# Kernel optimization log

Measured on AMD Instinct MI355X. Metric: run time of the kernel, lower is better.

The kernel has to match this reference:

```python
import jax, jax.numpy as jnp
import numpy as np

N = 129  # fixed by fc1: 3*121 -> N-8 = 121
F = 262144
E = 16384

def setup_inputs() -> dict:
    key = jax.random.key(0)
    ks = jax.random.split(key, 18)
    s = 0.05
    return {
        "x": jax.random.normal(ks[0], (N, F), jnp.float32),
        "edge_index": jax.random.randint(ks[1], (2, E), 0, N),
        "edge_attr": jax.random.uniform(ks[2], (E, 3), jnp.float32),
        # GCNConvSortPool (channel1 only; forward reuses it for all 3 edge channels)
        "gcn1_W": jax.random.normal(ks[3], (F, 1), jnp.float32) * (1.0 / np.sqrt(F)),
        "gcn1_b": jnp.zeros((1,), jnp.float32),
        "gcn2_W": jax.random.normal(ks[4], (1, 1), jnp.float32),
        "gcn2_b": jnp.zeros((1,), jnp.float32),
        "conv1_w": jax.random.normal(ks[5], (3, 2, 3), jnp.float32) * s,  # OIH
        "conv1_b": jax.random.normal(ks[6], (3,), jnp.float32) * s,
        "conv2_w": jax.random.normal(ks[7], (1, 3, 3), jnp.float32) * s,
        "conv2_b": jax.random.normal(ks[8], (1,), jnp.float32) * s,
        "fc1_W": jax.random.normal(ks[9], (3 * 121, 32), jnp.float32) * s,
        "fc1_b": jnp.zeros((32,), jnp.float32),
        "fc2_W": jax.random.normal(ks[10], (32, 6), jnp.float32) * s,
        "fc2_b": jnp.zeros((6,), jnp.float32),
        "fc3_W": jax.random.normal(ks[11], (6, 2), jnp.float32) * s,
        "fc3_b": jnp.zeros((2,), jnp.float32),
    }

def _gcn_conv(x, row, col, ew, W, b):
    # PyG GCNConv with edge weights: add self loops (weight 1), symmetric norm.
    n = x.shape[0]
    xw = x @ W                                             # [n, out]
    loop = jnp.arange(n)
    row2 = jnp.concatenate([row, loop])
    col2 = jnp.concatenate([col, loop])
    ew2 = jnp.concatenate([ew, jnp.ones((n,), x.dtype)])
    deg = jax.ops.segment_sum(ew2, col2, num_segments=n)
    dinv = jnp.where(deg > 0, deg ** -0.5, 0.0)
    norm = dinv[row2] * ew2 * dinv[col2]                   # [e+n]
    out = jax.ops.segment_sum(norm[:, None] * xw[row2], col2, num_segments=n)
    return out + b

def _maxpool1d3(z):
    return jax.lax.reduce_window(z, -jnp.inf, jax.lax.max, (1, 1, 3), (1, 1, 1), 'VALID')

def _conv1d(z, w, b):
    out = jax.lax.conv_general_dilated(z, w, (1,), 'VALID', dimension_numbers=('NCH', 'OIH', 'NCH'))
    return out + b[None, :, None]

def _channel(x, row, col, ew, gcn1_W, gcn1_b, gcn2_W, gcn2_b, conv1_w, conv1_b, conv2_w, conv2_b):
    h1 = _gcn_conv(x, row, col, ew, gcn1_W, gcn1_b)        # [N,1]
    h2 = _gcn_conv(h1[:, -1:], row, col, ew, gcn2_W, gcn2_b)  # [N,1]
    h = jnp.concatenate([h1, h2], axis=-1)                 # [N,2]
    perm = jnp.argsort(-h[:, -1])                          # SortPool: sort by last channel, descending, k=N
    h = h[perm]                                            # [N,2]
    z = h.T[None]                                          # [1,2,N]
    z = _maxpool1d3(_conv1d(z, conv1_w, conv1_b))          # [1,3,N-4]
    z = _maxpool1d3(_conv1d(z, conv2_w, conv2_b))          # [1,1,N-8]
    return z

def reference(x, edge_index, edge_attr, gcn1_W, gcn1_b, gcn2_W, gcn2_b,
              conv1_w, conv1_b, conv2_w, conv2_b,
              fc1_W, fc1_b, fc2_W, fc2_b, fc3_W, fc3_b):
    row, col = edge_index[0], edge_index[1]
    outs = [_channel(x, row, col, edge_attr[:, c], gcn1_W, gcn1_b, gcn2_W, gcn2_b,
                     conv1_w, conv1_b, conv2_w, conv2_b) for c in range(3)]
    all_x = jnp.concatenate(outs, axis=-2)                 # [1,3,121]
    h = all_x.reshape(1, -1)                               # [1,363]
    h = jax.nn.elu(h @ fc1_W + fc1_b)                      # dropout=0 -> identity
    h = jax.nn.elu(h @ fc2_W + fc2_b)
    return h @ fc3_W + fc3_b                               # [1,2]
```

## Files before the change

### kernel.cpp

```cpp
#include <hip/hip_runtime.h>
#include <hip/hip_bf16.h>
#include <math.h>

#define NN 129
#define FF 262144
#define EE 16384
#define CHUNKS 32
#define CHUNK (FF / CHUNKS)
#define NAGG 16
#define EPB (EE / NAGG)

#define OFF_PARTIAL 0
#define OFF_DEGP    (OFF_PARTIAL + NN*CHUNKS)
#define OFF_DINV    (OFF_DEGP + NAGG*3*NN)
#define OFF_XW      (OFF_DINV + 3*NN)
#define OFF_H1P     (OFF_XW + NN)
#define OFF_H1      (OFF_H1P + NAGG*3*NN)
#define OFF_H2P     (OFF_H1 + 3*NN)

__global__ __launch_bounds__(256) void k_matvec(
    const float* __restrict__ x, const float* __restrict__ W,
    const int* __restrict__ eidx, const float* __restrict__ eattr,
    double* __restrict__ ws)
{
    const int b = blockIdx.x;
    const int tid = threadIdx.x;
    const int wave = tid >> 6, lane = tid & 63;

    __shared__ double ws4[4];
    __shared__ double dp[4][3][NN];

    if (b < NN * CHUNKS) {
        const int r = b / CHUNKS, ch = b % CHUNKS;
        const float4* xp = (const float4*)(x + (size_t)r * FF + (size_t)ch * CHUNK);
        const float4* wp = (const float4*)(W + (size_t)ch * CHUNK);
        double acc = 0.0;
#pragma unroll
        for (int i = 0; i < CHUNK / (256 * 4); ++i) {
            float4 xv = xp[tid + i * 256];
            float4 wv = wp[tid + i * 256];
            acc += (double)xv.x * (double)wv.x + (double)xv.y * (double)wv.y
                 + (double)xv.z * (double)wv.z + (double)xv.w * (double)wv.w;
        }
        for (int off = 32; off > 0; off >>= 1) acc += __shfl_down(acc, off, 64);
        if (lane == 0) ws4[wave] = acc;
        __syncthreads();
        if (tid == 0) ws[OFF_PARTIAL + b] = (ws4[0] + ws4[1]) + (ws4[2] + ws4[3]);
    } else {
        const int bb = b - NN * CHUNKS;
        for (int i = tid; i < 4 * 3 * NN; i += 256) ((double*)dp)[i] = 0.0;
        __syncthreads();
        const int* col = eidx + EE;
#pragma unroll
        for (int i = 0; i < EPB / 256; ++i) {
            const int e = bb * EPB + i * 256 + tid;
            const int cl = col[e];
#pragma unroll
            for (int c = 0; c < 3; ++c)
                unsafeAtomicAdd(&dp[wave][c][cl], (double)eattr[e * 3 + c]);
        }
        __syncthreads();
        for (int i = tid; i < 3 * NN; i += 256)
            ws[OFF_DEGP + bb * (3 * NN) + i] =
                (dp[0][0][0 * 0] , ((dp[0][i / NN][i % NN] + dp[1][i / NN][i % NN])
                                  + (dp[2][i / NN][i % NN] + dp[3][i / NN][i % NN])));
    }
}

__global__ __launch_bounds__(256) void k_reduce1(double* __restrict__ ws)
{
    const int tid = threadIdx.x;
    if (blockIdx.x == 0) {
        for (int j = tid; j < NN; j += 256) {
            double s = 0.0;
#pragma unroll
            for (int k = 0; k < CHUNKS; ++k) s += ws[OFF_PARTIAL + j * CHUNKS + k];
            ws[OFF_XW + j] = s;
        }
    } else {
        for (int v = tid; v < 3 * NN; v += 256) {
            double d = 1.0;
#pragma unroll
            for (int b = 0; b < NAGG; ++b) d += ws[OFF_DEGP + b * (3 * NN) + v];
            ws[OFF_DINV + v] = (d > 0.0) ? 1.0 / sqrt(d) : 0.0;
        }
    }
}

__global__ __launch_bounds__(256) void k_agg1(
    const int* __restrict__ eidx, const float* __restrict__ eattr,
    double* __restrict__ ws)
{
    const int b = blockIdx.x, tid = threadIdx.x, wave = tid >> 6;
    __shared__ double sxw[NN];
    __shared__ double sdinv[3][NN];
    __shared__ double hp[4][3][NN];
    for (int i = tid; i < NN; i += 256) sxw[i] = ws[OFF_XW + i];
    for (int i = tid; i < 3 * NN; i += 256) ((double*)sdinv)[i] = ws[OFF_DINV + i];
    for (int i = tid; i < 4 * 3 * NN; i += 256) ((double*)hp)[i] = 0.0;
    __syncthreads();
    const int* row = eidx;
    const int* col = eidx + EE;
#pragma unroll
    for (int i = 0; i < EPB / 256; ++i) {
        const int e = b * EPB + i * 256 + tid;
        const int r = row[e], cl = col[e];
        const double xwr = sxw[r];
#pragma unroll
        for (int c = 0; c < 3; ++c) {
            const double nw = sdinv[c][r] * (double)eattr[e * 3 + c] * sdinv[c][cl];
            unsafeAtomicAdd(&hp[wave][c][cl], nw * xwr);
        }
    }
    __syncthreads();
    for (int i = tid; i < 3 * NN; i += 256) {
        const int c = i / NN, j = i % NN;
        ws[OFF_H1P + b * (3 * NN) + i] =
            (hp[0][c][j] + hp[1][c][j]) + (hp[2][c][j] + hp[3][c][j]);
    }
}

__global__ __launch_bounds__(256) void k_h1(
    const float* __restrict__ b1, double* __restrict__ ws)
{
    const int tid = threadIdx.x;
    const double bb1 = (double)b1[0];
    for (int i = tid; i < 3 * NN; i += 256) {
        const int j = i % NN;
        const double dv = ws[OFF_DINV + i];
        double s = dv * dv * ws[OFF_XW + j] + bb1;
#pragma unroll
        for (int b = 0; b < NAGG; ++b) s += ws[OFF_H1P + b * (3 * NN) + i];
        ws[OFF_H1 + i] = s;
    }
}

__global__ __launch_bounds__(256) void k_agg2(
    const int* __restrict__ eidx, const float* __restrict__ eattr,
    const float* __restrict__ W2, double* __restrict__ ws)
{
    const int b = blockIdx.x, tid = threadIdx.x, wave = tid >> 6;
    __shared__ double sh1[3][NN];
    __shared__ double sdinv[3][NN];
    __shared__ double hp[4][3][NN];
    const double w2 = (double)W2[0];
    for (int i = tid; i < 3 * NN; i += 256) {
        ((double*)sh1)[i] = ws[OFF_H1 + i];
        ((double*)sdinv)[i] = ws[OFF_DINV + i];
    }
    for (int i = tid; i < 4 * 3 * NN; i += 256) ((double*)hp)[i] = 0.0;
    __syncthreads();
    const int* row = eidx;
    const int* col = eidx + EE;
#pragma unroll
    for (int i = 0; i < EPB / 256; ++i) {
        const int e = b * EPB + i * 256 + tid;
        const int r = row[e], cl = col[e];
#pragma unroll
        for (int c = 0; c < 3; ++c) {
            const double nw = sdinv[c][r] * (double)eattr[e * 3 + c] * sdinv[c][cl];
            unsafeAtomicAdd(&hp[wave][c][cl], nw * (sh1[c][r] * w2));
        }
    }
    __syncthreads();
    for (int i = tid; i < 3 * NN; i += 256) {
        const int c = i / NN, j = i % NN;
        ws[OFF_H2P + b * (3 * NN) + i] =
            (hp[0][c][j] + hp[1][c][j]) + (hp[2][c][j] + hp[3][c][j]);
    }
}

__global__ __launch_bounds__(256) void k_final(
    const double* __restrict__ ws,
    const float* __restrict__ W2, const float* __restrict__ b2,
    const float* __restrict__ c1w, const float* __restrict__ c1b,
    const float* __restrict__ c2w, const float* __restrict__ c2b,
    const float* __restrict__ f1W, const float* __restrict__ f1b,
    const float* __restrict__ f2W, const float* __restrict__ f2b,
    const float* __restrict__ f3W, const float* __restrict__ f3b,
    float* __restrict__ out)
{
    __shared__ double h1[3][NN], h2[3][NN];
    __shared__ double z0[3][NN], z1[3][NN];
    __shared__ int    rnk[3][NN];
    __shared__ double c1o[3][3][127];
    __shared__ double p1o[3][3][125];
    __shared__ double c2o[3][123];
    __shared__ double allx[363];
    __shared__ double fc1o[32], fc2o[6];

    const int tid = threadIdx.x;
    const double w2 = (double)W2[0], bb2 = (double)b2[0];

    for (int i = tid; i < 3 * NN; i += 256) {
        const double hv = ws[OFF_H1 + i];
        ((double*)h1)[i] = hv;
        const double dv = ws[OFF_DINV + i];
        double s = dv * dv * (hv * w2) + bb2;
#pragma unroll
        for (int b = 0; b < NAGG; ++b) s += ws[OFF_H2P + b * (3 * NN) + i];
        ((double*)h2)[i] = s;
    }
    __syncthreads();

    for (int i = tid; i < 3 * NN; i += 256) {
        const int c = i / NN, j = i % NN;
        const double v = h2[c][j];
        int rk = 0;
        for (int q = 0; q < NN; ++q) {
            const double u = h2[c][q];
            rk += (u > v) || (u == v && q < j);
        }
        rnk[c][j] = rk;
    }
    __syncthreads();
    for (int i = tid; i < 3 * NN; i += 256) {
        const int c = i / NN, j = i % NN;
        const int rk = rnk[c][j];
        z0[c][rk] = h1[c][j];
        z1[c][rk] = h2[c][j];
    }
    __syncthreads();

    for (int i = tid; i < 3 * 3 * 127; i += 256) {
        const int c = i / (3 * 127), rem = i % (3 * 127), o = rem / 127, p = rem % 127;
        double s = (double)c1b[o];
#pragma unroll
        for (int k = 0; k < 3; ++k) {
            s += (double)c1w[(o * 2 + 0) * 3 + k] * z0[c][p + k];
            s += (double)c1w[(o * 2 + 1) * 3 + k] * z1[c][p + k];
        }
        c1o[c][o][p] = s;
    }
    __syncthreads();
    for (int i = tid; i < 3 * 3 * 125; i += 256) {
        const int c = i / (3 * 125), rem = i % (3 * 125), o = rem / 125, p = rem % 125;
        p1o[c][o][p] = fmax(c1o[c][o][p], fmax(c1o[c][o][p + 1], c1o[c][o][p + 2]));
    }
    __syncthreads();
    for (int i = tid; i < 3 * 123; i += 256) {
        const int c = i / 123, p = i % 123;
        double s = (double)c2b[0];
#pragma unroll
        for (int ic = 0; ic < 3; ++ic)
#pragma unroll
            for (int k = 0; k < 3; ++k)
                s += (double)c2w[ic * 3 + k] * p1o[c][ic][p + k];
        c2o[c][p] = s;
    }
    __syncthreads();
    for (int i = tid; i < 3 * 121; i += 256) {
        const int c = i / 121, p = i % 121;
        allx[c * 121 + p] = fmax(c2o[c][p], fmax(c2o[c][p + 1], c2o[c][p + 2]));
    }
    __syncthreads();

    {
        const int j = tid >> 3, t = tid & 7;
        double s = 0.0;
        for (int i = t; i < 363; i += 8) s += allx[i] * (double)f1W[i * 32 + j];
        s += __shfl_down(s, 4, 8);
        s += __shfl_down(s, 2, 8);
        s += __shfl_down(s, 1, 8);
        if (t == 0) {
            s += (double)f1b[j];
            fc1o[j] = (s > 0.0) ? s : expm1(s);
        }
    }
    __syncthreads();
    if (tid < 6) {
        double s = (double)f2b[tid];
        for (int i = 0; i < 32; ++i) s += fc1o[i] * (double)f2W[i * 6 + tid];
        fc2o[tid] = (s > 0.0) ? s : expm1(s);
    }
    __syncthreads();
    if (tid < 2) {
        double s = (double)f3b[tid];
        for (int i = 0; i < 6; ++i) s += fc2o[i] * (double)f3W[i * 2 + tid];
        out[tid] = (float)s;
    }
}

extern "C" void kernel_launch(void* const* d_in, const int* in_sizes, int n_in,
                              void* d_out, int out_size, void* d_ws, size_t ws_size,
                              hipStream_t stream) {
    const float* x    = (const float*)d_in[0];
    const int*   eidx = (const int*)d_in[1];
    const float* eattr= (const float*)d_in[2];
    const float* g1W  = (const float*)d_in[3];
    const float* g1b  = (const float*)d_in[4];
    const float* g2W  = (const float*)d_in[5];
    const float* g2b  = (const float*)d_in[6];
    const float* c1w  = (const float*)d_in[7];
    const float* c1b  = (const float*)d_in[8];
    const float* c2w  = (const float*)d_in[9];
    const float* c2b  = (const float*)d_in[10];
    const float* f1W  = (const float*)d_in[11];
    const float* f1b  = (const float*)d_in[12];
    const float* f2W  = (const float*)d_in[13];
    const float* f2b  = (const float*)d_in[14];
    const float* f3W  = (const float*)d_in[15];
    const float* f3b  = (const float*)d_in[16];
    float* out = (float*)d_out;
    double* ws = (double*)d_ws;

    k_matvec<<<NN * CHUNKS + NAGG, 256, 0, stream>>>(x, g1W, eidx, eattr, ws);
    k_reduce1<<<2, 256, 0, stream>>>(ws);
    k_agg1<<<NAGG, 256, 0, stream>>>(eidx, eattr, ws);
    k_h1<<<1, 256, 0, stream>>>(g1b, ws);
    k_agg2<<<NAGG, 256, 0, stream>>>(eidx, eattr, g2W, ws);
    k_final<<<1, 256, 0, stream>>>(ws, g2W, g2b, c1w, c1b, c2w, c2b,
                                   f1W, f1b, f2W, f2b, f3W, f3b, out);
}
```

Measured before the change: 266.0 us.

## Merge post-matvec stages into one kernel with software grid barriers

Folds reduce, both aggregation passes, the h1 combine and the final sort/conv/MLP stage into a single 16-block kernel. Two spin-wait barriers on atomics in global memory replace the kernel boundaries, and each block recomputes xw and dinv redundantly into shared memory. The goal is to cut launch and inter-kernel gap overhead from five small launches down to one. It relies on all 16 blocks being co-resident, and the barrier counters are reset by the previous kernel.

```diff
diff --git a/kernel.cpp b/kernel.cpp
--- a/kernel.cpp
+++ b/kernel.cpp
@@ -7,16 +7,14 @@
 #define EE 16384
 #define CHUNKS 32
 #define CHUNK (FF / CHUNKS)
-#define NAGG 16
-#define EPB (EE / NAGG)
+#define NB 16
+#define EPB (EE / NB)
 
 #define OFF_PARTIAL 0
 #define OFF_DEGP    (OFF_PARTIAL + NN*CHUNKS)
-#define OFF_DINV    (OFF_DEGP + NAGG*3*NN)
-#define OFF_XW      (OFF_DINV + 3*NN)
-#define OFF_H1P     (OFF_XW + NN)
-#define OFF_H1      (OFF_H1P + NAGG*3*NN)
-#define OFF_H2P     (OFF_H1 + 3*NN)
+#define OFF_H1P     (OFF_DEGP + NB*3*NN)
+#define OFF_H2P     (OFF_H1P + NB*3*NN)
+#define OFF_BAR     (OFF_H2P + NB*3*NN)
 
 __global__ __launch_bounds__(256) void k_matvec(
     const float* __restrict__ x, const float* __restrict__ W,
@@ -48,6 +46,11 @@
         if (tid == 0) ws[OFF_PARTIAL + b] = (ws4[0] + ws4[1]) + (ws4[2] + ws4[3]);
     } else {
         const int bb = b - NN * CHUNKS;
+        if (bb == 0 && tid == 0) {
+            unsigned* bar = (unsigned*)(ws + OFF_BAR);
+            __hip_atomic_store(&bar[0], 0u, __ATOMIC_RELAXED, __HIP_MEMORY_SCOPE_AGENT);
+            __hip_atomic_store(&bar[1], 0u, __ATOMIC_RELAXED, __HIP_MEMORY_SCOPE_AGENT);
+        }
         for (int i = tid; i < 4 * 3 * NN; i += 256) ((double*)dp)[i] = 0.0;
         __syncthreads();
         const int* col = eidx + EE;
@@ -60,119 +63,30 @@
                 unsafeAtomicAdd(&dp[wave][c][cl], (double)eattr[e * 3 + c]);
         }
         __syncthreads();
-        for (int i = tid; i < 3 * NN; i += 256)
+        for (int i = tid; i < 3 * NN; i += 256) {
+            const int c = i / NN, j = i % NN;
             ws[OFF_DEGP + bb * (3 * NN) + i] =
-                (dp[0][0][0 * 0] , ((dp[0][i / NN][i % NN] + dp[1][i / NN][i % NN])
-                                  + (dp[2][i / NN][i % NN] + dp[3][i / NN][i % NN])));
-    }
-}
-
-__global__ __launch_bounds__(256) void k_reduce1(double* __restrict__ ws)
-{
-    const int tid = threadIdx.x;
-    if (blockIdx.x == 0) {
-        for (int j = tid; j < NN; j += 256) {
-            double s = 0.0;
-#pragma unroll
-            for (int k = 0; k < CHUNKS; ++k) s += ws[OFF_PARTIAL + j * CHUNKS + k];
-            ws[OFF_XW + j] = s;
-        }
-    } else {
-        for (int v = tid; v < 3 * NN; v += 256) {
-            double d = 1.0;
-#pragma unroll
-            for (int b = 0; b < NAGG; ++b) d += ws[OFF_DEGP + b * (3 * NN) + v];
-            ws[OFF_DINV + v] = (d > 0.0) ? 1.0 / sqrt(d) : 0.0;
-        }
-    }
-}
-
-__global__ __launch_bounds__(256) void k_agg1(
+                (dp[0][c][j] + dp[1][c][j]) + (dp[2][c][j] + dp[3][c][j]);
+        }
+    }
+}
+
+__device__ __forceinline__ void gbar(unsigned* bar, int idx) {
+    __syncthreads();
+    if (threadIdx.x == 0) {
+        __threadfence();
+        __hip_atomic_fetch_add(&bar[idx], 1u, __ATOMIC_ACQ_REL, __HIP_MEMORY_SCOPE_AGENT);
+        while (__hip_atomic_load(&bar[idx], __ATOMIC_ACQUIRE, __HIP_MEMORY_SCOPE_AGENT) < (unsigned)NB)
+            __builtin_amdgcn_s_sleep(1);
+        __threadfence();
+    }
+    __syncthreads();
+}
+
+__global__ __launch_bounds__(256) void k_rest(
     const int* __restrict__ eidx, const float* __restrict__ eattr,
-    double* __restrict__ ws)
-{
-    const int b = blockIdx.x, tid = threadIdx.x, wave = tid >> 6;
-    __shared__ double sxw[NN];
-    __shared__ double sdinv[3][NN];
-    __shared__ double hp[4][3][NN];
-    for (int i = tid; i < NN; i += 256) sxw[i] = ws[OFF_XW + i];
-    for (int i = tid; i < 3 * NN; i += 256) ((double*)sdinv)[i] = ws[OFF_DINV + i];
-    for (int i = tid; i < 4 * 3 * NN; i += 256) ((double*)hp)[i] = 0.0;
-    __syncthreads();
-    const int* row = eidx;
-    const int* col = eidx + EE;
-#pragma unroll
-    for (int i = 0; i < EPB / 256; ++i) {
-        const int e = b * EPB + i * 256 + tid;
-        const int r = row[e], cl = col[e];
-        const double xwr = sxw[r];
-#pragma unroll
-        for (int c = 0; c < 3; ++c) {
-            const double nw = sdinv[c][r] * (double)eattr[e * 3 + c] * sdinv[c][cl];
-            unsafeAtomicAdd(&hp[wave][c][cl], nw * xwr);
-        }
-    }
-    __syncthreads();
-    for (int i = tid; i < 3 * NN; i += 256) {
-        const int c = i / NN, j = i % NN;
-        ws[OFF_H1P + b * (3 * NN) + i] =
-            (hp[0][c][j] + hp[1][c][j]) + (hp[2][c][j] + hp[3][c][j]);
-    }
-}
-
-__global__ __launch_bounds__(256) void k_h1(
-    const float* __restrict__ b1, double* __restrict__ ws)
-{
-    const int tid = threadIdx.x;
-    const double bb1 = (double)b1[0];
-    for (int i = tid; i < 3 * NN; i += 256) {
-        const int j = i % NN;
-        const double dv = ws[OFF_DINV + i];
-        double s = dv * dv * ws[OFF_XW + j] + bb1;
-#pragma unroll
-        for (int b = 0; b < NAGG; ++b) s += ws[OFF_H1P + b * (3 * NN) + i];
-        ws[OFF_H1 + i] = s;
-    }
-}
-
-__global__ __launch_bounds__(256) void k_agg2(
-    const int* __restrict__ eidx, const float* __restrict__ eattr,
-    const float* __restrict__ W2, double* __restrict__ ws)
-{
-    const int b = blockIdx.x, tid = threadIdx.x, wave = tid >> 6;
-    __shared__ double sh1[3][NN];
-    __shared__ double sdinv[3][NN];
-    __shared__ double hp[4][3][NN];
-    const double w2 = (double)W2[0];
-    for (int i = tid; i < 3 * NN; i += 256) {
-        ((double*)sh1)[i] = ws[OFF_H1 + i];
-        ((double*)sdinv)[i] = ws[OFF_DINV + i];
-    }
-    for (int i = tid; i < 4 * 3 * NN; i += 256) ((double*)hp)[i] = 0.0;
-    __syncthreads();
-    const int* row = eidx;
-    const int* col = eidx + EE;
-#pragma unroll
-    for (int i = 0; i < EPB / 256; ++i) {
-        const int e = b * EPB + i * 256 + tid;
-        const int r = row[e], cl = col[e];
-#pragma unroll
-        for (int c = 0; c < 3; ++c) {
-            const double nw = sdinv[c][r] * (double)eattr[e * 3 + c] * sdinv[c][cl];
-            unsafeAtomicAdd(&hp[wave][c][cl], nw * (sh1[c][r] * w2));
-        }
-    }
-    __syncthreads();
-    for (int i = tid; i < 3 * NN; i += 256) {
-        const int c = i / NN, j = i % NN;
-        ws[OFF_H2P + b * (3 * NN) + i] =
-            (hp[0][c][j] + hp[1][c][j]) + (hp[2][c][j] + hp[3][c][j]);
-    }
-}
-
-__global__ __launch_bounds__(256) void k_final(
-    const double* __restrict__ ws,
-    const float* __restrict__ W2, const float* __restrict__ b2,
+    double* __restrict__ ws,
+    const float* __restrict__ b1, const float* __restrict__ W2, const float* __restrict__ b2,
     const float* __restrict__ c1w, const float* __restrict__ c1b,
     const float* __restrict__ c2w, const float* __restrict__ c2b,
     const float* __restrict__ f1W, const float* __restrict__ f1b,
@@ -180,7 +94,11 @@
     const float* __restrict__ f3W, const float* __restrict__ f3b,
     float* __restrict__ out)
 {
-    __shared__ double h1[3][NN], h2[3][NN];
+    __shared__ double sxw[NN];
+    __shared__ double sdinv[3][NN];
+    __shared__ double sh1[3][NN];
+    __shared__ double hp[4][3][NN];
+    __shared__ double h2f[3][NN];
     __shared__ double z0[3][NN], z1[3][NN];
     __shared__ int    rnk[3][NN];
     __shared__ double c1o[3][3][127];
@@ -189,26 +107,95 @@
     __shared__ double allx[363];
     __shared__ double fc1o[32], fc2o[6];
 
-    const int tid = threadIdx.x;
-    const double w2 = (double)W2[0], bb2 = (double)b2[0];
-
-    for (int i = tid; i < 3 * NN; i += 256) {
-        const double hv = ws[OFF_H1 + i];
-        ((double*)h1)[i] = hv;
-        const double dv = ws[OFF_DINV + i];
-        double s = dv * dv * (hv * w2) + bb2;
-#pragma unroll
-        for (int b = 0; b < NAGG; ++b) s += ws[OFF_H2P + b * (3 * NN) + i];
-        ((double*)h2)[i] = s;
-    }
-    __syncthreads();
-
-    for (int i = tid; i < 3 * NN; i += 256) {
-        const int c = i / NN, j = i % NN;
-        const double v = h2[c][j];
+    const int b = blockIdx.x, tid = threadIdx.x, wave = tid >> 6;
+    unsigned* bar = (unsigned*)(ws + OFF_BAR);
+    const int* row = eidx;
+    const int* col = eidx + EE;
+
+    for (int j = tid; j < NN; j += 256) {
+        double s = 0.0;
+#pragma unroll
+        for (int k = 0; k < CHUNKS; ++k) s += ws[OFF_PARTIAL + j * CHUNKS + k];
+        sxw[j] = s;
+    }
+    for (int v = tid; v < 3 * NN; v += 256) {
+        double d = 1.0;
+#pragma unroll
+        for (int k = 0; k < NB; ++k) d += ws[OFF_DEGP + k * (3 * NN) + v];
+        ((double*)sdinv)[v] = (d > 0.0) ? 1.0 / sqrt(d) : 0.0;
+    }
+    for (int i = tid; i < 4 * 3 * NN; i += 256) ((double*)hp)[i] = 0.0;
+    __syncthreads();
+
+#pragma unroll
+    for (int i = 0; i < EPB / 256; ++i) {
+        const int e = b * EPB + i * 256 + tid;
+        const int r = row[e], cl = col[e];
+        const double xwr = sxw[r];
+#pragma unroll
+        for (int c = 0; c < 3; ++c) {
+            const double nw = sdinv[c][r] * (double)eattr[e * 3 + c] * sdinv[c][cl];
+            unsafeAtomicAdd(&hp[wave][c][cl], nw * xwr);
+        }
+    }
+    __syncthreads();
+    for (int i = tid; i < 3 * NN; i += 256) {
+        const int c = i / NN, j = i % NN;
+        ws[OFF_H1P + b * (3 * NN) + i] =
+            (hp[0][c][j] + hp[1][c][j]) + (hp[2][c][j] + hp[3][c][j]);
+    }
+    gbar(bar, 0);
+
+    const double bb1 = (double)b1[0];
+    for (int i = tid; i < 3 * NN; i += 256) {
+        const int j = i % NN;
+        const double dv = ((double*)sdinv)[i];
+        double s = dv * dv * sxw[j] + bb1;
+#pragma unroll
+        for (int k = 0; k < NB; ++k) s += ws[OFF_H1P + k * (3 * NN) + i];
+        ((double*)sh1)[i] = s;
+    }
+    for (int i = tid; i < 4 * 3 * NN; i += 256) ((double*)hp)[i] = 0.0;
+    __syncthreads();
+
+    const double w2 = (double)W2[0];
+#pragma unroll
+    for (int i = 0; i < EPB / 256; ++i) {
+        const int e = b * EPB + i * 256 + tid;
+        const int r = row[e], cl = col[e];
+#pragma unroll
+        for (int c = 0; c < 3; ++c) {
+            const double nw = sdinv[c][r] * (double)eattr[e * 3 + c] * sdinv[c][cl];
+            unsafeAtomicAdd(&hp[wave][c][cl], nw * (sh1[c][r] * w2));
+        }
+    }
+    __syncthreads();
+    for (int i = tid; i < 3 * NN; i += 256) {
+        const int c = i / NN, j = i % NN;
+        ws[OFF_H2P + b * (3 * NN) + i] =
+            (hp[0][c][j] + hp[1][c][j]) + (hp[2][c][j] + hp[3][c][j]);
+    }
+    gbar(bar, 1);
+
+    if (b != 0) return;
+
+    const double bb2 = (double)b2[0];
+    for (int i = tid; i < 3 * NN; i += 256) {
+        const int j = i % NN;
+        const double dv = ((double*)sdinv)[i];
+        double s = dv * dv * (((double*)sh1)[i] * w2) + bb2;
+#pragma unroll
+        for (int k = 0; k < NB; ++k) s += ws[OFF_H2P + k * (3 * NN) + i];
+        ((double*)h2f)[i] = s;
+    }
+    __syncthreads();
+
+    for (int i = tid; i < 3 * NN; i += 256) {
+        const int c = i / NN, j = i % NN;
+        const double v = h2f[c][j];
         int rk = 0;
         for (int q = 0; q < NN; ++q) {
-            const double u = h2[c][q];
+            const double u = h2f[c][q];
             rk += (u > v) || (u == v && q < j);
         }
         rnk[c][j] = rk;
@@ -217,8 +204,8 @@
     for (int i = tid; i < 3 * NN; i += 256) {
         const int c = i / NN, j = i % NN;
         const int rk = rnk[c][j];
-        z0[c][rk] = h1[c][j];
-        z1[c][rk] = h2[c][j];
+        z0[c][rk] = sh1[c][j];
+        z1[c][rk] = h2f[c][j];
     }
     __syncthreads();
 
@@ -304,11 +291,8 @@
     float* out = (float*)d_out;
     double* ws = (double*)d_ws;
 
-    k_matvec<<<NN * CHUNKS + NAGG, 256, 0, stream>>>(x, g1W, eidx, eattr, ws);
-    k_reduce1<<<2, 256, 0, stream>>>(ws);
-    k_agg1<<<NAGG, 256, 0, stream>>>(eidx, eattr, ws);
-    k_h1<<<1, 256, 0, stream>>>(g1b, ws);
-    k_agg2<<<NAGG, 256, 0, stream>>>(eidx, eattr, g2W, ws);
-    k_final<<<1, 256, 0, stream>>>(ws, g2W, g2b, c1w, c1b, c2w, c2b,
+    k_matvec<<<NN * CHUNKS + NB, 256, 0, stream>>>(x, g1W, eidx, eattr, ws);
+    k_rest<<<NB, 256, 0, stream>>>(eidx, eattr, ws,
+                                   g1b, g2W, g2b, c1w, c1b, c2w, c2b,
                                    f1W, f1b, f2W, f2b, f3W, f3b, out);
 }
```

Measured after the change: 265.2 us. About the same (-0.3%).
